# Performance work log

Measured on AMD Instinct MI355X. Metric: run time of the kernel, lower is better.

Reference implementation:

```python
import jax, jax.numpy as jnp
import numpy as np
from jax import lax

N = 2_097_152  # batch of FP16 numbers
BITS = 16

# MSB-first bit weights: [S, E4..E0, M9..M0] -> bit i has weight 2^(15-i)
_WEIGHTS = (2 ** jnp.arange(15, -1, -1, dtype=jnp.int32)).astype(jnp.uint32)
_SHIFTS = jnp.arange(15, -1, -1, dtype=jnp.uint32)


def bits_to_f16(bits):
    """bits: [..., 16] float 0/1 spikes (MSB first) -> float16 values [...]."""
    u = jnp.sum(bits.astype(jnp.uint32) * _WEIGHTS, axis=-1).astype(jnp.uint16)
    return lax.bitcast_convert_type(u, jnp.float16)


def f16_to_bits(x):
    """float16 [...] -> [..., 16] float32 0/1 spikes (MSB first)."""
    u = lax.bitcast_convert_type(x, jnp.uint16).astype(jnp.uint32)
    return ((u[..., None] >> _SHIFTS) & 1).astype(jnp.float32)


def setup_inputs() -> dict:
    key = jax.random.key(0)
    kA, kB = jax.random.split(key)
    # Random FP16 bit patterns encoded as 0/1 float spikes, MSB first.
    A = jax.random.randint(kA, (N, BITS), 0, 2).astype(jnp.float32)
    B = jax.random.randint(kB, (N, BITS), 0, 2).astype(jnp.float32)
    return {"A": A, "B": B}


def reference(A, B):
    """Spiking gate-network FP16 adder == IEEE-754 binary16 addition (RNE)
    on the bit-encoded operands. Decode spikes -> fp16, add, re-encode.
    This computes the same function as the AND/OR/XOR/MUX gate network
    (align shift, mantissa add/sub, LZD normalize, round, overflow/NaN),
    expressed as one fused vectorized op.
    """
    fa = bits_to_f16(A)
    fb = bits_to_f16(B)
    s = fa + fb  # IEEE fp16 add, round-to-nearest-even
    return f16_to_bits(s)
```

## Files before the change

kernel.cpp:

```cpp
#include <hip/hip_runtime.h>
#include <stdint.h>

__device__ __forceinline__ float h2f(uint32_t h) {
    uint32_t s = (h & 0x8000u) << 16;
    uint32_t e = (h >> 10) & 0x1fu;
    uint32_t m = h & 0x3ffu;
    if (e == 0) {
        float v = (float)m * 5.9604644775390625e-08f;
        return __uint_as_float(s | __float_as_uint(v));
    }
    uint32_t fb;
    if (e == 31) fb = s | 0x7f800000u | (m << 13);
    else         fb = s | ((e + 112u) << 23) | (m << 13);
    return __uint_as_float(fb);
}

__device__ __forceinline__ uint32_t f2h(uint32_t f) {
    uint32_t h_sgn = (f & 0x80000000u) >> 16;
    uint32_t f_exp = f & 0x7f800000u;
    uint32_t f_sig;

    if (f_exp >= 0x47800000u) {
        if (f_exp == 0x7f800000u) {
            f_sig = f & 0x007fffffu;
            if (f_sig != 0u) {
                uint32_t ret = 0x7c00u + (f_sig >> 13);
                if (ret == 0x7c00u) ret++;
                return h_sgn + ret;
            }
            return h_sgn + 0x7c00u;
        }
        return h_sgn + 0x7c00u;
    }

    if (f_exp <= 0x38000000u) {
        if (f_exp < 0x33000000u) return h_sgn;
        uint32_t fe = f_exp >> 23;
        f_sig = 0x00800000u + (f & 0x007fffffu);
        f_sig >>= (113u - fe);
        if (((f_sig & 0x00003fffu) != 0x00001000u) || (f & 0x000007ffu)) {
            f_sig += 0x00001000u;
        }
        return h_sgn + (f_sig >> 13);
    }

    uint32_t h_exp = (f_exp - 0x38000000u) >> 13;
    f_sig = f & 0x007fffffu;
    if ((f_sig & 0x00003fffu) != 0x00001000u) {
        f_sig += 0x00001000u;
    }
    uint32_t h_sig = f_sig >> 13;
    return h_sgn + h_exp + h_sig;
}

__device__ __forceinline__ uint32_t pack4(uint4 c, uint32_t u, int top) {
    u |= ((c.x >> 23) & 1u) << top;
    u |= ((c.y >> 23) & 1u) << (top - 1);
    u |= ((c.z >> 23) & 1u) << (top - 2);
    u |= ((c.w >> 23) & 1u) << (top - 3);
    return u;
}

__device__ __forceinline__ uint4 unpack4(uint32_t r, int top) {
    uint4 o;
    o.x = ((r >> top)       & 1u) * 0x3f800000u;
    o.y = ((r >> (top - 1)) & 1u) * 0x3f800000u;
    o.z = ((r >> (top - 2)) & 1u) * 0x3f800000u;
    o.w = ((r >> (top - 3)) & 1u) * 0x3f800000u;
    return o;
}

__global__ __launch_bounds__(256) void spike_fp16_add_kernel(
    const uint4* __restrict__ A, const uint4* __restrict__ B,
    uint4* __restrict__ O, int rows)
{
    int i = blockIdx.x * blockDim.x + threadIdx.x;
    if (i >= rows) return;

    const uint4* ap = A + (size_t)i * 4;
    const uint4* bp = B + (size_t)i * 4;

    uint4 a0 = ap[0], a1 = ap[1], a2 = ap[2], a3 = ap[3];
    uint4 b0 = bp[0], b1 = bp[1], b2 = bp[2], b3 = bp[3];

    uint32_t ua = 0, ub = 0;
    ua = pack4(a0, ua, 15); ua = pack4(a1, ua, 11);
    ua = pack4(a2, ua, 7);  ua = pack4(a3, ua, 3);
    ub = pack4(b0, ub, 15); ub = pack4(b1, ub, 11);
    ub = pack4(b2, ub, 7);  ub = pack4(b3, ub, 3);

    uint32_t ea = ua & 0x7fffu;
    uint32_t eb = ub & 0x7fffu;

    float fa = h2f(ua);
    float fb = h2f(ub);
    uint32_t r = f2h(__float_as_uint(fa + fb));

    if (ea == 0x7c00u && (ua ^ ub) == 0x8000u) r = 0xfe00u;
    if (eb > 0x7c00u) r = ub | 0x0200u;
    if (ea > 0x7c00u) r = ua | 0x0200u;

    uint4* op = O + (size_t)i * 4;
    op[0] = unpack4(r, 15);
    op[1] = unpack4(r, 11);
    op[2] = unpack4(r, 7);
    op[3] = unpack4(r, 3);
}

extern "C" void kernel_launch(void* const* d_in, const int* in_sizes, int n_in,
                              void* d_out, int out_size, void* d_ws, size_t ws_size,
                              hipStream_t stream) {
    const uint4* A = (const uint4*)d_in[0];
    const uint4* B = (const uint4*)d_in[1];
    uint4* O = (uint4*)d_out;
    int rows = in_sizes[0] / 16;
    int threads = 256;
    int blocks = (rows + threads - 1) / threads;
    spike_fp16_add_kernel<<<blocks, threads, 0, stream>>>(A, B, O, rows);
}
```

Baseline: 308.4 us.

## Coalesce loads by splitting each row across four lanes with shuffle-OR

```diff
diff --git a/kernel.cpp b/kernel.cpp
--- a/kernel.cpp
+++ b/kernel.cpp
@@ -1,5 +1,6 @@
 #include <hip/hip_runtime.h>
 #include <stdint.h>
+
 
 __device__ __forceinline__ float h2f(uint32_t h) {
     uint32_t s = (h & 0x8000u) << 16;
@@ -53,7 +54,19 @@
     return h_sgn + h_exp + h_sig;
 }
 
-__device__ __forceinline__ uint32_t pack4(uint4 c, uint32_t u, int top) {
+__device__ __forceinline__ uint32_t fp16_add(uint32_t ua, uint32_t ub) {
+    uint32_t ea = ua & 0x7fffu;
+    uint32_t eb = ub & 0x7fffu;
+    uint32_t r = f2h(__float_as_uint(h2f(ua) + h2f(ub)));
+    if (ea == 0x7c00u && (ua ^ ub) == 0x8000u) r = 0xfe00u;
+    if (eb > 0x7c00u) r = ub | 0x0200u;
+    if (ea > 0x7c00u) r = ua | 0x0200u;
+    return r;
+}
+
+
+__device__ __forceinline__ uint32_t pack4(uint4 c, int top) {
+    uint32_t u = 0;
     u |= ((c.x >> 23) & 1u) << top;
     u |= ((c.y >> 23) & 1u) << (top - 1);
     u |= ((c.z >> 23) & 1u) << (top - 2);
@@ -70,41 +83,48 @@
     return o;
 }
 
+__device__ __forceinline__ uint32_t orreduce4(uint32_t v) {
+    v |= __shfl_xor(v, 1, 64);
+    v |= __shfl_xor(v, 2, 64);
+    return v;
+}
+
 __global__ __launch_bounds__(256) void spike_fp16_add_kernel(
     const uint4* __restrict__ A, const uint4* __restrict__ B,
-    uint4* __restrict__ O, int rows)
+    uint4* __restrict__ O)
 {
-    int i = blockIdx.x * blockDim.x + threadIdx.x;
-    if (i >= rows) return;
+    const int t = threadIdx.x;
+    const int c = t & 3;
+    const int top = 15 - 4 * c;
+    const size_t base = (size_t)blockIdx.x * 1024;
 
-    const uint4* ap = A + (size_t)i * 4;
-    const uint4* bp = B + (size_t)i * 4;
+    uint4 a0 = A[base + t];
+    uint4 a1 = A[base + t + 256];
+    uint4 a2 = A[base + t + 512];
+    uint4 a3 = A[base + t + 768];
+    uint4 b0 = B[base + t];
+    uint4 b1 = B[base + t + 256];
+    uint4 b2 = B[base + t + 512];
+    uint4 b3 = B[base + t + 768];
 
-    uint4 a0 = ap[0], a1 = ap[1], a2 = ap[2], a3 = ap[3];
-    uint4 b0 = bp[0], b1 = bp[1], b2 = bp[2], b3 = bp[3];
+    uint32_t ua0 = orreduce4(pack4(a0, top));
+    uint32_t ua1 = orreduce4(pack4(a1, top));
+    uint32_t ua2 = orreduce4(pack4(a2, top));
+    uint32_t ua3 = orreduce4(pack4(a3, top));
+    uint32_t ub0 = orreduce4(pack4(b0, top));
+    uint32_t ub1 = orreduce4(pack4(b1, top));
+    uint32_t ub2 = orreduce4(pack4(b2, top));
+    uint32_t ub3 = orreduce4(pack4(b3, top));
 
-    uint32_t ua = 0, ub = 0;
-    ua = pack4(a0, ua, 15); ua = pack4(a1, ua, 11);
-    ua = pack4(a2, ua, 7);  ua = pack4(a3, ua, 3);
-    ub = pack4(b0, ub, 15); ub = pack4(b1, ub, 11);
-    ub = pack4(b2, ub, 7);  ub = pack4(b3, ub, 3);
+    uint32_t r0 = fp16_add(ua0, ub0);
+    uint32_t r1 = fp16_add(ua1, ub1);
+    uint32_t r2 = fp16_add(ua2, ub2);
+    uint32_t r3 = fp16_add(ua3, ub3);
 
-    uint32_t ea = ua & 0x7fffu;
-    uint32_t eb = ub & 0x7fffu;
-
-    float fa = h2f(ua);
-    float fb = h2f(ub);
-    uint32_t r = f2h(__float_as_uint(fa + fb));
-
-    if (ea == 0x7c00u && (ua ^ ub) == 0x8000u) r = 0xfe00u;
-    if (eb > 0x7c00u) r = ub | 0x0200u;
-    if (ea > 0x7c00u) r = ua | 0x0200u;
-
-    uint4* op = O + (size_t)i * 4;
-    op[0] = unpack4(r, 15);
-    op[1] = unpack4(r, 11);
-    op[2] = unpack4(r, 7);
-    op[3] = unpack4(r, 3);
+    O[base + t]       = unpack4(r0, top);
+    O[base + t + 256] = unpack4(r1, top);
+    O[base + t + 512] = unpack4(r2, top);
+    O[base + t + 768] = unpack4(r3, top);
 }
 
 extern "C" void kernel_launch(void* const* d_in, const int* in_sizes, int n_in,
@@ -114,7 +134,6 @@
     const uint4* B = (const uint4*)d_in[1];
     uint4* O = (uint4*)d_out;
     int rows = in_sizes[0] / 16;
-    int threads = 256;
-    int blocks = (rows + threads - 1) / threads;
-    spike_fp16_add_kernel<<<blocks, threads, 0, stream>>>(A, B, O, rows);
+    int blocks = rows / 256;
+    spike_fp16_add_kernel<<<blocks, 256, 0, stream>>>(A, B, O);
 }
```

New measurement: 305.5 us. About the same (-1.0%).
